# Kernel optimization log

Measured on AMD Instinct MI355X. Metric: run time of the kernel, lower is better.

The kernel has to match this reference:

```python
import jax, jax.numpy as jnp
import numpy as np

W_ENTROPY, W_MI, W_COV, W_ORTHO, W_L1, W_L2 = 1.0, 0.2, 0.2, 0.1, 0.1, 0.1


def setup_inputs() -> dict:
    key = jax.random.key(0)
    k1, k2, k3, k4 = jax.random.split(key, 4)
    B, NCLS, C = 16384, 1000, 1280
    logits = jax.random.normal(k1, (B, NCLS), dtype=jnp.float32)
    output = jax.nn.log_softmax(logits, axis=1)  # nll_loss expects log-probs
    target = jax.random.randint(k2, (B,), 0, NCLS, dtype=jnp.int64)
    weights = jax.random.normal(k3, (NCLS, C), dtype=jnp.float32) * 0.02
    features = jax.random.normal(k4, (B, C), dtype=jnp.float32)
    return {"output": output, "target": target, "weights": weights, "features": features}


def _kl_loss(features):
    # torch: sum_{i,j} F.kl_div(L[:, i], L[:, j], log_target=True, reduction='mean')
    # kl_div(input, tgt, log_target=True) = mean_b exp(tgt)*(tgt - input)
    # => sum_{i,j,b} P[b,j]*(L[b,j]-L[b,i]) / B
    #  = (C * sum(P*L) - sum(L)) / B   (since sum_j P[b,j] == 1)
    B, C = features.shape
    L = jax.nn.log_softmax(features, axis=1)
    P = jnp.exp(L)
    return (C * jnp.sum(P * L) - jnp.sum(L)) / B


def _cov_loss(features):
    B = features.shape[0]
    cf = features - jnp.mean(features, axis=0, keepdims=True)
    cov = (cf.T @ cf) / B  # [C, C]
    eye = jnp.eye(cov.shape[0], dtype=cov.dtype)
    return jnp.sum((cov - eye) ** 2)  # ||.||_F^2


def _ortho_loss(weights):
    w = weights.reshape(weights.shape[0], -1)
    cov = w @ w.T  # row type
    eye = jnp.eye(cov.shape[0], dtype=cov.dtype)
    return jnp.sum((cov - eye) ** 2)


def reference(output, target, weights, features):
    loss_nll = -jnp.mean(jnp.take_along_axis(output, target[:, None], axis=1))
    loss_kl = _kl_loss(features)
    loss_cov = _cov_loss(features)
    loss_ortho = _ortho_loss(weights)
    loss_l1 = jnp.sum(jnp.abs(weights))
    loss_l2 = jnp.sqrt(jnp.sum(weights ** 2))
    loss = (W_ENTROPY * loss_nll + W_MI * loss_kl + W_COV * loss_cov
            + W_ORTHO * loss_ortho + W_L1 * loss_l1 + W_L2 * loss_l2)
    return loss
```

## Files before the change

kernel.cpp:

```cpp
#include <hip/hip_runtime.h>
#include <stdint.h>
#include <stddef.h>

#define B_N    16384
#define NCLS_N 1000
#define C_N    1280

#define ACC_OFF    0ULL
#define TICKET_OFF 64ULL
#define COLSUM_OFF 128ULL
#define FBT_OFF    8192ULL
#define WB_OFF     41951232ULL
#define G_OFF      44572672ULL
#define H_OFF      51126272ULL

enum { A_NLL = 0, A_KL = 1, A_L1 = 2, A_L2SQ = 3, A_SUMSQF = 4, A_FMU2 = 5, A_GFRO = 6, A_HFRO = 7 };

typedef short s16x8 __attribute__((ext_vector_type(8)));
typedef float f32x4 __attribute__((ext_vector_type(4)));

__device__ __forceinline__ unsigned short f2bf(float f) {
    union { float f; unsigned int u; } v; v.f = f;
    unsigned int u = v.u;
    u += 0x7fffu + ((u >> 16) & 1u);
    return (unsigned short)(u >> 16);
}

__device__ __forceinline__ float wave_red(float v) {
#pragma unroll
    for (int o = 32; o; o >>= 1) v += __shfl_down(v, o, 64);
    return v;
}


__device__ __forceinline__ void nll_body(const float* __restrict__ lp,
                                         const int* __restrict__ tgt,
                                         float* __restrict__ acc, int bidx) {
    int b = bidx * 256 + threadIdx.x;
    int t = tgt[b];
    float v = lp[(size_t)b * NCLS_N + t];
    v = wave_red(v);
    __shared__ float sm_nll[4];
    int wid = threadIdx.x >> 6, lane = threadIdx.x & 63;
    if (lane == 0) sm_nll[wid] = v;
    __syncthreads();
    if (threadIdx.x == 0) atomicAdd(&acc[A_NLL], sm_nll[0] + sm_nll[1] + sm_nll[2] + sm_nll[3]);
}

__device__ __forceinline__ void wpass_body(const float* __restrict__ W,
                                           short* __restrict__ Wb,
                                           float* __restrict__ acc, int idx) {
    int bx = idx & 3;
    int kc = idx >> 2;
    int m = bx * 256 + threadIdx.x;
    bool live = (m < NCLS_N);
    const float4* Wr = (const float4*)(W + (size_t)m * C_N);
    float l1 = 0.f, l2 = 0.f;
#pragma unroll
    for (int kj = 0; kj < 4; kj++) {
        s16x8 pk = { 0, 0, 0, 0, 0, 0, 0, 0 };
        if (live) {
            float4 a = Wr[kc * 8 + kj * 2];
            float4 b = Wr[kc * 8 + kj * 2 + 1];
            l1 += fabsf(a.x) + fabsf(a.y) + fabsf(a.z) + fabsf(a.w)
                + fabsf(b.x) + fabsf(b.y) + fabsf(b.z) + fabsf(b.w);
            l2 += a.x * a.x + a.y * a.y + a.z * a.z + a.w * a.w
                + b.x * b.x + b.y * b.y + b.z * b.z + b.w * b.w;
            pk[0] = (short)f2bf(a.x); pk[1] = (short)f2bf(a.y);
            pk[2] = (short)f2bf(a.z); pk[3] = (short)f2bf(a.w);
            pk[4] = (short)f2bf(b.x); pk[5] = (short)f2bf(b.y);
            pk[6] = (short)f2bf(b.z); pk[7] = (short)f2bf(b.w);
        }
        *(s16x8*)(Wb + ((size_t)(kc * 4 + kj) * 1024 + m) * 8) = pk;
    }
    l1 = wave_red(l1);
    l2 = wave_red(l2);
    __shared__ float sm_w[4][2];
    int wid = threadIdx.x >> 6, lane = threadIdx.x & 63;
    if (lane == 0) { sm_w[wid][0] = l1; sm_w[wid][1] = l2; }
    __syncthreads();
    if (threadIdx.x == 0) {
        atomicAdd(&acc[A_L1],   sm_w[0][0] + sm_w[1][0] + sm_w[2][0] + sm_w[3][0]);
        atomicAdd(&acc[A_L2SQ], sm_w[0][1] + sm_w[1][1] + sm_w[2][1] + sm_w[3][1]);
    }
}

__device__ __forceinline__ void fpass_body(const float* __restrict__ F,
                                           short* __restrict__ Fbt,
                                           float* __restrict__ colsum,
                                           float* __restrict__ acc, int idx) {
    int bx = idx % 5;
    int by = idx / 5;
    int c = bx * 256 + threadIdx.x;
    int kc0 = by * 4;
    float cs = 0.f, sq = 0.f;
    for (int ch = 0; ch < 4; ch++) {
        int kc = kc0 + ch;
        int kbase = kc * 32;
#pragma unroll
        for (int kj = 0; kj < 4; kj++) {
            float v[8];
#pragma unroll
            for (int e = 0; e < 8; e++) v[e] = F[(size_t)(kbase + kj * 8 + e) * C_N + c];
            s16x8 pk;
#pragma unroll
            for (int e = 0; e < 8; e++) {
                cs += v[e];
                sq += v[e] * v[e];
                pk[e] = (short)f2bf(v[e]);
            }
            *(s16x8*)(Fbt + ((size_t)(kc * 4 + kj) * C_N + c) * 8) = pk;
        }
    }
    atomicAdd(&colsum[c], cs);
    sq = wave_red(sq);
    __shared__ float sm_f[4];
    int wid = threadIdx.x >> 6, lane = threadIdx.x & 63;
    if (lane == 0) sm_f[wid] = sq;
    __syncthreads();
    if (threadIdx.x == 0) atomicAdd(&acc[A_SUMSQF], sm_f[0] + sm_f[1] + sm_f[2] + sm_f[3]);
}

__device__ __forceinline__ void klpass_body(const float* __restrict__ F,
                                            const float* __restrict__ colsum,
                                            float* __restrict__ acc, int idx) {
    int wid = threadIdx.x >> 6, lane = threadIdx.x & 63;
    int gwave = idx * 4 + wid;
    const float4* M = (const float4*)colsum;

    float kl_acc = 0.f, fmu_acc = 0.f;
    for (int b = gwave; b < B_N; b += 4096) {
        const float4* Fr = (const float4*)(F + (size_t)b * C_N);
        float s = 0.f, tt = 0.f, sf = 0.f, dp = 0.f;
#pragma unroll
        for (int i = 0; i < 5; i++) {
            float4 f = Fr[lane + 64 * i];
            float4 m = M[lane + 64 * i];
            float e0 = __expf(f.x), e1 = __expf(f.y), e2 = __expf(f.z), e3 = __expf(f.w);
            s  += e0 + e1 + e2 + e3;
            tt += e0 * f.x + e1 * f.y + e2 * f.z + e3 * f.w;
            sf += f.x + f.y + f.z + f.w;
            dp += f.x * m.x + f.y * m.y + f.z * m.z + f.w * m.w;
        }
        s = wave_red(s); tt = wave_red(tt); sf = wave_red(sf); dp = wave_red(dp);
        if (lane == 0) {
            kl_acc += (float)C_N * (tt / s) - sf;
            float dot = dp * (1.f / (float)B_N);
            fmu_acc += dot * dot;
        }
    }
    __shared__ float sm_kl[4][2];
    if (lane == 0) { sm_kl[wid][0] = kl_acc; sm_kl[wid][1] = fmu_acc; }
    __syncthreads();
    if (threadIdx.x == 0) {
        atomicAdd(&acc[A_KL],   sm_kl[0][0] + sm_kl[1][0] + sm_kl[2][0] + sm_kl[3][0]);
        atomicAdd(&acc[A_FMU2], sm_kl[0][1] + sm_kl[1][1] + sm_kl[2][1] + sm_kl[3][1]);
    }
}

__device__ __forceinline__ void gram_body(const short* __restrict__ X,
                                          float* __restrict__ S,
                                          int Mp, int T, int tile, int kc_blk, int chunkK) {
    __shared__ __align__(16) short A0[128 * 32];
    __shared__ __align__(16) short A1[128 * 32];
    __shared__ __align__(16) short B0[128 * 32];
    __shared__ __align__(16) short B1[128 * 32];
    int tid = threadIdx.x;
    int bi = 0, rem = tile;
    while (rem >= T - bi) { rem -= T - bi; bi++; }
    int bj = bi + rem;
    int i0 = bi * 128, j0 = bj * 128;
    bool same = (bi == bj);

    int wave = tid >> 6, lane = tid & 63;
    int wm = wave >> 1, wn = wave & 1;
    int quad = lane >> 4, l16 = lane & 15;

    const size_t kstep = (size_t)Mp * 32;
    const short *pa0, *pa1, *pb0, *pb1;
    int lo0 = tid * 8, lo1 = (256 + tid) * 8;
    {
        int g0 = tid, g1 = 256 + tid;
        int r0 = g0 >> 2, r1 = g1 >> 2;
        int kj0 = (g0 & 3) ^ (r0 & 3), kj1 = (g1 & 3) ^ (r1 & 3);
        size_t base = (size_t)(kc_blk * chunkK >> 5) * kstep;
        pa0 = X + base + ((size_t)kj0 * Mp + i0 + r0) * 8;
        pa1 = X + base + ((size_t)kj1 * Mp + i0 + r1) * 8;
        pb0 = X + base + ((size_t)kj0 * Mp + j0 + r0) * 8;
        pb1 = X + base + ((size_t)kj1 * Mp + j0 + r1) * 8;
    }

    f32x4 acc[4][4];
#pragma unroll
    for (int i = 0; i < 4; i++)
#pragma unroll
        for (int j = 0; j < 4; j++) acc[i][j] = { 0.f, 0.f, 0.f, 0.f };

    auto stage = [&](short* Ad, short* Bd) {
        __builtin_amdgcn_global_load_lds((const __attribute__((address_space(1))) unsigned int*)pa0,
                                         (__attribute__((address_space(3))) unsigned int*)(Ad + lo0), 16, 0, 0);
        __builtin_amdgcn_global_load_lds((const __attribute__((address_space(1))) unsigned int*)pa1,
                                         (__attribute__((address_space(3))) unsigned int*)(Ad + lo1), 16, 0, 0);
        if (!same) {
            __builtin_amdgcn_global_load_lds((const __attribute__((address_space(1))) unsigned int*)pb0,
                                             (__attribute__((address_space(3))) unsigned int*)(Bd + lo0), 16, 0, 0);
            __builtin_amdgcn_global_load_lds((const __attribute__((address_space(1))) unsigned int*)pb1,
                                             (__attribute__((address_space(3))) unsigned int*)(Bd + lo1), 16, 0, 0);
        }
        pa0 += kstep; pa1 += kstep; pb0 += kstep; pb1 += kstep;
    };

    auto compute = [&](const short* Ab, const short* Bb) {
        s16x8 af[4], bfr[4];
#pragma unroll
        for (int f = 0; f < 4; f++) {
            int mrow = wm * 64 + f * 16 + l16;
            af[f] = *(const s16x8*)(Ab + mrow * 32 + (quad ^ (mrow & 3)) * 8);
            int nrow = wn * 64 + f * 16 + l16;
            bfr[f] = *(const s16x8*)(Bb + nrow * 32 + (quad ^ (nrow & 3)) * 8);
        }
        __builtin_amdgcn_s_setprio(1);
#pragma unroll
        for (int i = 0; i < 4; i++)
#pragma unroll
            for (int j = 0; j < 4; j++)
                acc[i][j] = __builtin_amdgcn_mfma_f32_16x16x32_bf16(af[i], bfr[j], acc[i][j], 0, 0, 0);
        __builtin_amdgcn_s_setprio(0);
    };

    int nt = chunkK >> 5;
    stage(A0, B0);
    __syncthreads();
    for (int t = 0; t < nt; t += 2) {
        stage(A1, B1);
        compute(A0, same ? A0 : B0);
        __syncthreads();
        if (t + 2 < nt) stage(A0, B0);
        compute(A1, same ? A1 : B1);
        __syncthreads();
    }

#pragma unroll
    for (int i = 0; i < 4; i++)
#pragma unroll
        for (int j = 0; j < 4; j++)
#pragma unroll
            for (int r = 0; r < 4; r++) {
                int grow = i0 + wm * 64 + i * 16 + quad * 4 + r;
                int gcol = j0 + wn * 64 + j * 16 + l16;
                atomicAdd(&S[(size_t)grow * Mp + gcol], acc[i][j][r]);
            }
}

__device__ __forceinline__ void fro_tile(const float* __restrict__ S,
                                         int Mp, int T, int tile, float* __restrict__ slot) {
    int bi = 0, rem = tile;
    while (rem >= T - bi) { rem -= T - bi; bi++; }
    int bj = bi + rem;
    size_t base = (size_t)bi * 128 * Mp + (size_t)bj * 128;
    float sum = 0.f;
    for (int l = threadIdx.x * 4; l < 128 * 128; l += 1024) {
        int row = l >> 7, col = l & 127;
        float4 v = *(const float4*)(S + base + (size_t)row * Mp + col);
        sum += v.x * v.x + v.y * v.y + v.z * v.z + v.w * v.w;
    }
    sum = wave_red(sum);
    __shared__ float sm_fro[4];
    int wid = threadIdx.x >> 6, lane = threadIdx.x & 63;
    if (lane == 0) sm_fro[wid] = sum;
    __syncthreads();
    if (threadIdx.x == 0) {
        float w = (bi == bj) ? 1.f : 2.f;
        atomicAdd(slot, w * (sm_fro[0] + sm_fro[1] + sm_fro[2] + sm_fro[3]));
    }
}


__global__ __launch_bounds__(256) void prep_kernel(const float* __restrict__ lp,
                                                   const int* __restrict__ tgt,
                                                   const float* __restrict__ W,
                                                   const float* __restrict__ F,
                                                   short* __restrict__ Wb,
                                                   short* __restrict__ Fbt,
                                                   float* __restrict__ colsum,
                                                   float* __restrict__ acc,
                                                   float* __restrict__ G,
                                                   float* __restrict__ H) {
    int b = blockIdx.x;
    if (b < 640) {
        fpass_body(F, Fbt, colsum, acc, b);
    } else if (b < 800) {
        wpass_body(W, Wb, acc, b - 640);
    } else if (b < 864) {
        nll_body(lp, tgt, acc, b - 800);
    } else if (b < 964) {
        float4* p = (float4*)G + (size_t)(b - 864) * 4096;
        float4 z = { 0.f, 0.f, 0.f, 0.f };
        for (int i = threadIdx.x; i < 4096; i += 256) p[i] = z;
    } else {
        float4* p = (float4*)H + (size_t)(b - 964) * 4096;
        float4 z = { 0.f, 0.f, 0.f, 0.f };
        for (int i = threadIdx.x; i < 4096; i += 256) p[i] = z;
    }
}

__global__ __launch_bounds__(256) void main_kernel(const short* __restrict__ Fbt,
                                                   float* __restrict__ G,
                                                   const short* __restrict__ Wb,
                                                   float* __restrict__ H,
                                                   const float* __restrict__ F,
                                                   const float* __restrict__ colsum,
                                                   float* __restrict__ acc) {
    int b = blockIdx.x;
    if (b < 880) {
        gram_body(Fbt, G, C_N, 10, b >> 4, b & 15, 1024);
    } else if (b < 1904) {
        klpass_body(F, colsum, acc, b - 880);
    } else {
        int l = b - 1904;
        gram_body(Wb, H, 1024, 8, l >> 2, l & 3, 320);
    }
}

__global__ __launch_bounds__(256) void fro_final_kernel(const float* __restrict__ G,
                                                        const float* __restrict__ H,
                                                        float* __restrict__ acc,
                                                        const float* __restrict__ colsum,
                                                        unsigned* __restrict__ ticket,
                                                        float* __restrict__ out) {
    int b = blockIdx.x;
    if (b < 55) fro_tile(G, C_N, 10, b, acc + A_GFRO);
    else        fro_tile(H, 1024, 8, b - 55, acc + A_HFRO);

    __shared__ int amlast;
    if (threadIdx.x == 0) {
        __threadfence();
        unsigned prev = atomicAdd(ticket, 1u);
        amlast = (prev == 90u);
    }
    __syncthreads();
    if (!amlast) return;
    __threadfence();

    float s = 0.f;
    for (int c = threadIdx.x; c < C_N; c += 256) { float v = colsum[c]; s += v * v; }
    s = wave_red(s);
    __shared__ float sm[4];
    int wid = threadIdx.x >> 6, lane = threadIdx.x & 63;
    if (lane == 0) sm[wid] = s;
    __syncthreads();
    if (threadIdx.x == 0) {
        double musq_raw = (double)(sm[0] + sm[1] + sm[2] + sm[3]);
        double Bd = (double)B_N;
        double gfro = (double)atomicAdd(&acc[A_GFRO], 0.0f);
        double hfro = (double)atomicAdd(&acc[A_HFRO], 0.0f);
        double nll = -((double)acc[A_NLL] / Bd);
        double kl  = (double)acc[A_KL] / Bd;
        double trG = (double)acc[A_SUMSQF];
        double musq = musq_raw / (Bd * Bd);
        double cov = gfro / (Bd * Bd)
                   - (2.0 / Bd) * (double)acc[A_FMU2]
                   + musq * musq
                   - 2.0 * (trG / Bd - musq)
                   + (double)C_N;
        double ortho = hfro - 2.0 * (double)acc[A_L2SQ] + (double)NCLS_N;
        double loss = 1.0 * nll + 0.2 * kl + 0.2 * cov + 0.1 * ortho
                    + 0.1 * (double)acc[A_L1] + 0.1 * sqrt((double)acc[A_L2SQ]);
        out[0] = (float)loss;
    }
}

extern "C" void kernel_launch(void* const* d_in, const int* in_sizes, int n_in,
                              void* d_out, int out_size, void* d_ws, size_t ws_size,
                              hipStream_t stream) {
    (void)in_sizes; (void)n_in; (void)out_size; (void)ws_size;
    const float* output_lp = (const float*)d_in[0];
    const int*   target    = (const int*)d_in[1];
    const float* W         = (const float*)d_in[2];
    const float* F         = (const float*)d_in[3];

    char*     ws     = (char*)d_ws;
    float*    acc    = (float*)(ws + ACC_OFF);
    unsigned* ticket = (unsigned*)(ws + TICKET_OFF);
    float*    colsum = (float*)(ws + COLSUM_OFF);
    short*    Fbt    = (short*)(ws + FBT_OFF);
    short*    Wb     = (short*)(ws + WB_OFF);
    float*    G      = (float*)(ws + G_OFF);
    float*    H      = (float*)(ws + H_OFF);

    hipMemsetAsync(ws, 0, 8192, stream);

    prep_kernel<<<1028, 256, 0, stream>>>(output_lp, target, W, F, Wb, Fbt, colsum, acc, G, H);
    main_kernel<<<2048, 256, 0, stream>>>(Fbt, G, Wb, H, F, colsum, acc);
    fro_final_kernel<<<91, 256, 0, stream>>>(G, H, acc, colsum, ticket, (float*)d_out);
}
```

Baseline: 297.2 us.

## Compute mu^T G mu term from Gram tiles and move KL pass to prep kernel

The per-row dot product of features with the column mean (the FMU2 term) is replaced by an equivalent quadratic form mu^T G mu, evaluated while the Frobenius pass reads the Gram tiles. This lets the KL pass drop its colsum dependency, so it moves from the main kernel into the prep kernel alongside the other F-reading work. The main kernel then only runs Gram GEMMs. The Gram body also drops its same-tile shortcut and always loads the B operand, which simplifies the code but adds redundant loads on diagonal tiles.

```diff
diff --git a/kernel.cpp b/kernel.cpp
--- a/kernel.cpp
+++ b/kernel.cpp
@@ -122,40 +122,29 @@
 }
 
 __device__ __forceinline__ void klpass_body(const float* __restrict__ F,
-                                            const float* __restrict__ colsum,
                                             float* __restrict__ acc, int idx) {
     int wid = threadIdx.x >> 6, lane = threadIdx.x & 63;
     int gwave = idx * 4 + wid;
-    const float4* M = (const float4*)colsum;
-
-    float kl_acc = 0.f, fmu_acc = 0.f;
+    float kl_acc = 0.f;
     for (int b = gwave; b < B_N; b += 4096) {
         const float4* Fr = (const float4*)(F + (size_t)b * C_N);
-        float s = 0.f, tt = 0.f, sf = 0.f, dp = 0.f;
+        float s = 0.f, tt = 0.f, sf = 0.f;
 #pragma unroll
         for (int i = 0; i < 5; i++) {
             float4 f = Fr[lane + 64 * i];
-            float4 m = M[lane + 64 * i];
             float e0 = __expf(f.x), e1 = __expf(f.y), e2 = __expf(f.z), e3 = __expf(f.w);
             s  += e0 + e1 + e2 + e3;
             tt += e0 * f.x + e1 * f.y + e2 * f.z + e3 * f.w;
             sf += f.x + f.y + f.z + f.w;
-            dp += f.x * m.x + f.y * m.y + f.z * m.z + f.w * m.w;
-        }
-        s = wave_red(s); tt = wave_red(tt); sf = wave_red(sf); dp = wave_red(dp);
-        if (lane == 0) {
-            kl_acc += (float)C_N * (tt / s) - sf;
-            float dot = dp * (1.f / (float)B_N);
-            fmu_acc += dot * dot;
-        }
-    }
-    __shared__ float sm_kl[4][2];
-    if (lane == 0) { sm_kl[wid][0] = kl_acc; sm_kl[wid][1] = fmu_acc; }
-    __syncthreads();
-    if (threadIdx.x == 0) {
-        atomicAdd(&acc[A_KL],   sm_kl[0][0] + sm_kl[1][0] + sm_kl[2][0] + sm_kl[3][0]);
-        atomicAdd(&acc[A_FMU2], sm_kl[0][1] + sm_kl[1][1] + sm_kl[2][1] + sm_kl[3][1]);
-    }
+        }
+        s = wave_red(s); tt = wave_red(tt); sf = wave_red(sf);
+        if (lane == 0) kl_acc += (float)C_N * (tt / s) - sf;
+    }
+    __shared__ float sm_kl[4];
+    if (lane == 0) sm_kl[wid] = kl_acc;
+    __syncthreads();
+    if (threadIdx.x == 0)
+        atomicAdd(&acc[A_KL], sm_kl[0] + sm_kl[1] + sm_kl[2] + sm_kl[3]);
 }
 
 __device__ __forceinline__ void gram_body(const short* __restrict__ X,
@@ -170,7 +159,6 @@
     while (rem >= T - bi) { rem -= T - bi; bi++; }
     int bj = bi + rem;
     int i0 = bi * 128, j0 = bj * 128;
-    bool same = (bi == bj);
 
     int wave = tid >> 6, lane = tid & 63;
     int wm = wave >> 1, wn = wave & 1;
@@ -201,12 +189,10 @@
                                          (__attribute__((address_space(3))) unsigned int*)(Ad + lo0), 16, 0, 0);
         __builtin_amdgcn_global_load_lds((const __attribute__((address_space(1))) unsigned int*)pa1,
                                          (__attribute__((address_space(3))) unsigned int*)(Ad + lo1), 16, 0, 0);
-        if (!same) {
-            __builtin_amdgcn_global_load_lds((const __attribute__((address_space(1))) unsigned int*)pb0,
-                                             (__attribute__((address_space(3))) unsigned int*)(Bd + lo0), 16, 0, 0);
-            __builtin_amdgcn_global_load_lds((const __attribute__((address_space(1))) unsigned int*)pb1,
-                                             (__attribute__((address_space(3))) unsigned int*)(Bd + lo1), 16, 0, 0);
-        }
+        __builtin_amdgcn_global_load_lds((const __attribute__((address_space(1))) unsigned int*)pb0,
+                                         (__attribute__((address_space(3))) unsigned int*)(Bd + lo0), 16, 0, 0);
+        __builtin_amdgcn_global_load_lds((const __attribute__((address_space(1))) unsigned int*)pb1,
+                                         (__attribute__((address_space(3))) unsigned int*)(Bd + lo1), 16, 0, 0);
         pa0 += kstep; pa1 += kstep; pb0 += kstep; pb1 += kstep;
     };
 
@@ -233,10 +219,10 @@
     __syncthreads();
     for (int t = 0; t < nt; t += 2) {
         stage(A1, B1);
-        compute(A0, same ? A0 : B0);
+        compute(A0, B0);
         __syncthreads();
         if (t + 2 < nt) stage(A0, B0);
-        compute(A1, same ? A1 : B1);
+        compute(A1, B1);
         __syncthreads();
     }
 
@@ -253,25 +239,37 @@
 }
 
 __device__ __forceinline__ void fro_tile(const float* __restrict__ S,
-                                         int Mp, int T, int tile, float* __restrict__ slot) {
+                                         const float* __restrict__ mu_src,
+                                         int Mp, int T, int tile,
+                                         float* __restrict__ slotF,
+                                         float* __restrict__ slotQ) {
     int bi = 0, rem = tile;
     while (rem >= T - bi) { rem -= T - bi; bi++; }
     int bj = bi + rem;
     size_t base = (size_t)bi * 128 * Mp + (size_t)bj * 128;
-    float sum = 0.f;
+    const float invB = 1.f / (float)B_N;
+    float sum = 0.f, q = 0.f;
     for (int l = threadIdx.x * 4; l < 128 * 128; l += 1024) {
         int row = l >> 7, col = l & 127;
         float4 v = *(const float4*)(S + base + (size_t)row * Mp + col);
         sum += v.x * v.x + v.y * v.y + v.z * v.z + v.w * v.w;
+        if (mu_src) {
+            float mr = mu_src[bi * 128 + row] * invB;
+            float4 mc = *(const float4*)(mu_src + bj * 128 + col);
+            q += mr * (v.x * mc.x + v.y * mc.y + v.z * mc.z + v.w * mc.w) * invB;
+        }
     }
     sum = wave_red(sum);
-    __shared__ float sm_fro[4];
-    int wid = threadIdx.x >> 6, lane = threadIdx.x & 63;
-    if (lane == 0) sm_fro[wid] = sum;
+    q = wave_red(q);
+    __shared__ float sm_fro[4][2];
+    int wid = threadIdx.x >> 6, lane = threadIdx.x & 63;
+    if (lane == 0) { sm_fro[wid][0] = sum; sm_fro[wid][1] = q; }
     __syncthreads();
     if (threadIdx.x == 0) {
         float w = (bi == bj) ? 1.f : 2.f;
-        atomicAdd(slot, w * (sm_fro[0] + sm_fro[1] + sm_fro[2] + sm_fro[3]));
+        atomicAdd(slotF, w * (sm_fro[0][0] + sm_fro[1][0] + sm_fro[2][0] + sm_fro[3][0]));
+        if (mu_src)
+            atomicAdd(slotQ, w * (sm_fro[0][1] + sm_fro[1][1] + sm_fro[2][1] + sm_fro[3][1]));
     }
 }
 
@@ -287,18 +285,20 @@
                                                    float* __restrict__ G,
                                                    float* __restrict__ H) {
     int b = blockIdx.x;
-    if (b < 640) {
-        fpass_body(F, Fbt, colsum, acc, b);
-    } else if (b < 800) {
-        wpass_body(W, Wb, acc, b - 640);
-    } else if (b < 864) {
-        nll_body(lp, tgt, acc, b - 800);
-    } else if (b < 964) {
-        float4* p = (float4*)G + (size_t)(b - 864) * 4096;
+    if (b < 1024) {
+        klpass_body(F, acc, b);
+    } else if (b < 1664) {
+        fpass_body(F, Fbt, colsum, acc, b - 1024);
+    } else if (b < 1824) {
+        wpass_body(W, Wb, acc, b - 1664);
+    } else if (b < 1888) {
+        nll_body(lp, tgt, acc, b - 1824);
+    } else if (b < 1988) {
+        float4* p = (float4*)G + (size_t)(b - 1888) * 4096;
         float4 z = { 0.f, 0.f, 0.f, 0.f };
         for (int i = threadIdx.x; i < 4096; i += 256) p[i] = z;
     } else {
-        float4* p = (float4*)H + (size_t)(b - 964) * 4096;
+        float4* p = (float4*)H + (size_t)(b - 1988) * 4096;
         float4 z = { 0.f, 0.f, 0.f, 0.f };
         for (int i = threadIdx.x; i < 4096; i += 256) p[i] = z;
     }
@@ -307,17 +307,12 @@
 __global__ __launch_bounds__(256) void main_kernel(const short* __restrict__ Fbt,
                                                    float* __restrict__ G,
                                                    const short* __restrict__ Wb,
-                                                   float* __restrict__ H,
-                                                   const float* __restrict__ F,
-                                                   const float* __restrict__ colsum,
-                                                   float* __restrict__ acc) {
+                                                   float* __restrict__ H) {
     int b = blockIdx.x;
     if (b < 880) {
         gram_body(Fbt, G, C_N, 10, b >> 4, b & 15, 1024);
-    } else if (b < 1904) {
-        klpass_body(F, colsum, acc, b - 880);
     } else {
-        int l = b - 1904;
+        int l = b - 880;
         gram_body(Wb, H, 1024, 8, l >> 2, l & 3, 320);
     }
 }
@@ -329,8 +324,8 @@
                                                         unsigned* __restrict__ ticket,
                                                         float* __restrict__ out) {
     int b = blockIdx.x;
-    if (b < 55) fro_tile(G, C_N, 10, b, acc + A_GFRO);
-    else        fro_tile(H, 1024, 8, b - 55, acc + A_HFRO);
+    if (b < 55) fro_tile(G, colsum, C_N, 10, b, acc + A_GFRO, acc + A_FMU2);
+    else        fro_tile(H, nullptr, 1024, 8, b - 55, acc + A_HFRO, nullptr);
 
     __shared__ int amlast;
     if (threadIdx.x == 0) {
@@ -354,12 +349,13 @@
         double Bd = (double)B_N;
         double gfro = (double)atomicAdd(&acc[A_GFRO], 0.0f);
         double hfro = (double)atomicAdd(&acc[A_HFRO], 0.0f);
+        double fmu2 = (double)atomicAdd(&acc[A_FMU2], 0.0f);
         double nll = -((double)acc[A_NLL] / Bd);
         double kl  = (double)acc[A_KL] / Bd;
         double trG = (double)acc[A_SUMSQF];
         double musq = musq_raw / (Bd * Bd);
         double cov = gfro / (Bd * Bd)
-                   - (2.0 / Bd) * (double)acc[A_FMU2]
+                   - (2.0 / Bd) * fmu2
                    + musq * musq
                    - 2.0 * (trG / Bd - musq)
                    + (double)C_N;
@@ -390,7 +386,7 @@
 
     hipMemsetAsync(ws, 0, 8192, stream);
 
-    prep_kernel<<<1028, 256, 0, stream>>>(output_lp, target, W, F, Wb, Fbt, colsum, acc, G, H);
-    main_kernel<<<2048, 256, 0, stream>>>(Fbt, G, Wb, H, F, colsum, acc);
+    prep_kernel<<<2052, 256, 0, stream>>>(output_lp, target, W, F, Wb, Fbt, colsum, acc, G, H);
+    main_kernel<<<1024, 256, 0, stream>>>(Fbt, G, Wb, H);
     fro_final_kernel<<<91, 256, 0, stream>>>(G, H, acc, colsum, ticket, (float*)d_out);
 }
```

Result: no change. 294.9 us (-0.8%).
